# Optimization experiments

Hardware: AMD Instinct MI355X
Metric: run time of the kernel (lower is better)

## Reference

```python
import jax, jax.numpy as jnp
import numpy as np

B, N, IN_F, OUT_F, H = 4, 2048, 128, 128, 4
D = OUT_F // H  # head_dim = 32
NEG_SLOPE = 0.2


def setup_inputs() -> dict:
    key = jax.random.key(0)
    k1, k2, k3, k4, k5 = jax.random.split(key, 5)
    x = jax.random.normal(k1, (B, N, IN_F), dtype=jnp.float32)
    adj = jax.random.randint(k2, (N, N), 0, 2, dtype=jnp.int32)
    adj = adj.at[jnp.arange(N), jnp.arange(N)].set(1)  # self-loops
    # xavier-uniform-like init
    lim_w = float(np.sqrt(6.0 / (IN_F + OUT_F)))
    W = jax.random.uniform(k3, (OUT_F, IN_F), minval=-lim_w, maxval=lim_w, dtype=jnp.float32)
    lim_a = float(np.sqrt(6.0 / (H + D)))
    a_src = jax.random.uniform(k4, (H, D), minval=-lim_a, maxval=lim_a, dtype=jnp.float32)
    a_dst = jax.random.uniform(k5, (H, D), minval=-lim_a, maxval=lim_a, dtype=jnp.float32)
    return {"x": x, "adj": adj, "W": W, "a_src": a_src, "a_dst": a_dst}


def reference(x, adj, W, a_src, a_dst):
    Bx, Nx, _ = x.shape
    # linear projection: (B,N,out) -> (B,N,H,D)
    h = jnp.einsum('bni,oi->bno', x, W).reshape(Bx, Nx, H, D)
    e_src = jnp.einsum('bnhd,hd->bnh', h, a_src)  # (B,N,H)
    e_dst = jnp.einsum('bnhd,hd->bnh', h, a_dst)  # (B,N,H)
    # scores: (B,N_src,H,N_dst)
    scores = jax.nn.leaky_relu(
        e_src[:, :, :, None] + e_dst.transpose(0, 2, 1)[:, None, :, :],
        negative_slope=NEG_SLOPE,
    )
    mask = adj[None, :, None, :]  # (1,N,1,N)
    scores = jnp.where(mask == 0, -jnp.inf, scores)
    attn = jax.nn.softmax(scores, axis=-1)  # (B,N,H,N); dropout is identity at eval
    out = jnp.einsum('bnhm,bmhd->bnhd', attn, h)  # (B,N,H,D)
    return out.reshape(Bx, Nx, H * D)
```

## Files before the change

kernel.cpp:

```cpp
#include <hip/hip_runtime.h>
#include <math.h>

#define BB 4
#define NN 2048
#define FF 128
#define HH 4
#define DD 32
#define NEG_SLOPE 0.2f
#define LOG2E 1.4426950408889634f

typedef __attribute__((ext_vector_type(8))) short short8;
typedef __attribute__((ext_vector_type(4))) float floatx4;
typedef __attribute__((ext_vector_type(2))) float floatx2;

__device__ __forceinline__ float exp2_fast(float x) {
#if __has_builtin(__builtin_amdgcn_exp2f)
    return __builtin_amdgcn_exp2f(x);
#else
    return exp2f(x);
#endif
}

__device__ __forceinline__ int bit_mask(unsigned int w, int bit) {
#if __has_builtin(__builtin_amdgcn_sbfe)
    return __builtin_amdgcn_sbfe((int)w, bit, 1);
#else
    return ((int)(w << (31 - bit))) >> 31;
#endif
}

__device__ __forceinline__ unsigned int pack2_rtne(float lo, float hi) {
    unsigned int ul = __float_as_uint(lo); ul += 0x7FFFu + ((ul >> 16) & 1u);
    unsigned int uh = __float_as_uint(hi); uh += 0x7FFFu + ((uh >> 16) & 1u);
    return (ul >> 16) | (uh & 0xFFFF0000u);
}

__global__ __launch_bounds__(256) void k_prep(const float* __restrict__ x,
                                              const float* __restrict__ W,
                                              const float* __restrict__ a_src,
                                              const float* __restrict__ a_dst,
                                              const int* __restrict__ adj,
                                              unsigned short* __restrict__ ht,
                                              float* __restrict__ es_t,
                                              float* __restrict__ ed_t,
                                              unsigned int* __restrict__ bits) {
    __shared__ unsigned short wbf[128][144];
    __shared__ unsigned short hbf[128][24];
    __shared__ float vs_s[HH][FF], vd_s[HH][FF];
    __shared__ float as_s[FF], ad_s[FF];
    int t = threadIdx.x;

    if (blockIdx.x >= 512) {
        int idx = (blockIdx.x - 512) * 256 + t;
        int n = idx >> 6, w = idx & 63;
        const int4* base = (const int4*)(adj + (size_t)n * NN + w * 32);
        unsigned int word = 0;
#pragma unroll
        for (int q = 0; q < 8; ++q) {
            int4 a = base[q];
            word |= ((unsigned int)(a.x & 1)) << (q * 4 + 0);
            word |= ((unsigned int)(a.y & 1)) << (q * 4 + 1);
            word |= ((unsigned int)(a.z & 1)) << (q * 4 + 2);
            word |= ((unsigned int)(a.w & 1)) << (q * 4 + 3);
        }
        bits[idx] = word;
        return;
    }

    int m0g = blockIdx.x * 16;
    int b = m0g >> 11;
    int m_block = m0g & 2047;

    if (t < FF) { as_s[t] = a_src[t]; ad_s[t] = a_dst[t]; }
#pragma unroll
    for (int k = 0; k < 8; ++k) {
        int idx = t + k * 256;
        int row = idx >> 4, ch = idx & 15;
        const float* wp = W + (size_t)row * FF + ch * 8;
        float4 v0 = *(const float4*)wp;
        float4 v1 = *(const float4*)(wp + 4);
        unsigned int u[4];
        u[0] = pack2_rtne(v0.x, v0.y); u[1] = pack2_rtne(v0.z, v0.w);
        u[2] = pack2_rtne(v1.x, v1.y); u[3] = pack2_rtne(v1.z, v1.w);
        *(int4*)&wbf[row][ch * 8] = *(const int4*)u;
    }
    __syncthreads();

    {
        int i = t & 127;
        float acc4[4] = {0.f, 0.f, 0.f, 0.f};
        if (t < 128) {
            for (int o = 0; o < 128; ++o) {
                float wv = __uint_as_float(((unsigned int)wbf[o][i]) << 16);
                acc4[o >> 5] += wv * as_s[o];
            }
#pragma unroll
            for (int hd = 0; hd < 4; ++hd) vs_s[hd][i] = acc4[hd];
        } else {
            for (int o = 0; o < 128; ++o) {
                float wv = __uint_as_float(((unsigned int)wbf[o][i]) << 16);
                acc4[o >> 5] += wv * ad_s[o];
            }
#pragma unroll
            for (int hd = 0; hd < 4; ++hd) vd_s[hd][i] = acc4[hd];
        }
    }

    int wid = t >> 6, lane = t & 63;
    int r = lane & 15, q = lane >> 4;
    floatx4 acc[2] = {{0.f,0.f,0.f,0.f},{0.f,0.f,0.f,0.f}};
    const float* xrow = x + (size_t)(m0g + r) * FF + q * 8;
#pragma unroll
    for (int kk = 0; kk < 4; ++kk) {
        float4 a0 = *(const float4*)(xrow + kk * 32);
        float4 a1 = *(const float4*)(xrow + kk * 32 + 4);
        union { short8 s8; unsigned int u[4]; } af;
        af.u[0] = pack2_rtne(a0.x, a0.y); af.u[1] = pack2_rtne(a0.z, a0.w);
        af.u[2] = pack2_rtne(a1.x, a1.y); af.u[3] = pack2_rtne(a1.z, a1.w);
#pragma unroll
        for (int c = 0; c < 2; ++c) {
            int o = (wid * 2 + c) * 16 + r;
            short8 bf = *(const short8*)&wbf[o][kk * 32 + q * 8];
            acc[c] = __builtin_amdgcn_mfma_f32_16x16x32_bf16(af.s8, bf, acc[c], 0, 0, 0);
        }
    }
#pragma unroll
    for (int c = 0; c < 2; ++c) {
        int o = (wid * 2 + c) * 16 + r;
        unsigned int u2[2];
        u2[0] = pack2_rtne(acc[c][0], acc[c][1]);
        u2[1] = pack2_rtne(acc[c][2], acc[c][3]);
        *(int2*)&hbf[o][q * 4] = *(const int2*)u2;
    }
    __syncthreads();

    if (t < 128) {
        int hd = t >> 5, d = t & 31;
        unsigned short* op = ht + ((size_t)(b * HH + hd) * DD + d) * NN + m_block;
        *(int4*)op       = *(const int4*)&hbf[t][0];
        *(int4*)(op + 8) = *(const int4*)&hbf[t][8];
    }
    {
        int m = t >> 4, sg = t & 15;
        const float* xp = x + (size_t)(m0g + m) * FF + sg * 8;
        float4 x0 = *(const float4*)xp;
        float4 x1 = *(const float4*)(xp + 4);
#pragma unroll
        for (int hd = 0; hd < 4; ++hd) {
            const float* vsp = &vs_s[hd][sg * 8];
            const float* vdp = &vd_s[hd][sg * 8];
            float es = x0.x * vsp[0] + x0.y * vsp[1] + x0.z * vsp[2] + x0.w * vsp[3]
                     + x1.x * vsp[4] + x1.y * vsp[5] + x1.z * vsp[6] + x1.w * vsp[7];
            float ed = x0.x * vdp[0] + x0.y * vdp[1] + x0.z * vdp[2] + x0.w * vdp[3]
                     + x1.x * vdp[4] + x1.y * vdp[5] + x1.z * vdp[6] + x1.w * vdp[7];
#pragma unroll
            for (int k = 1; k < 16; k <<= 1) {
                es += __shfl_xor(es, k);
                ed += __shfl_xor(ed, k);
            }
            if (sg == 0) {
                size_t eb = (size_t)(b * HH + hd) * NN + m_block + m;
                es_t[eb] = es * LOG2E;
                ed_t[eb] = ed * LOG2E;
            }
        }
    }
}

__global__ __launch_bounds__(512) void k_attn(
        const unsigned short* __restrict__ ht,
        const unsigned int* __restrict__ bits,
        const float* __restrict__ es_t,
        const float* __restrict__ ed_t,
        float* __restrict__ out) {
    __shared__ float ep[NN * 2];
    int t = threadIdx.x;
    int n0 = blockIdx.x * 64;
    int bh = blockIdx.y;
    int b = bh >> 2, head = bh & 3;

    int wid = t >> 6, lane = t & 63;
    int q = lane >> 4, r = lane & 15;
    int qo = q * 8;
    int half = wid >> 2, wsub = wid & 3;
    int n_l = wsub * 16 + r;

    {
        float4 v = ((const float4*)(ed_t + (size_t)bh * NN))[t];
        float4 o01, o23;
        o01.x = exp2_fast(v.x); o01.y = exp2_fast(NEG_SLOPE * v.x);
        o01.z = exp2_fast(v.y); o01.w = exp2_fast(NEG_SLOPE * v.y);
        o23.x = exp2_fast(v.z); o23.y = exp2_fast(NEG_SLOPE * v.z);
        o23.z = exp2_fast(v.w); o23.w = exp2_fast(NEG_SLOPE * v.w);
        ((float4*)ep)[2 * t]     = o01;
        ((float4*)ep)[2 * t + 1] = o23;
    }
    float esv = es_t[(size_t)bh * NN + n0 + n_l];
    floatx2 es2 = {exp2_fast(esv), exp2_fast(NEG_SLOPE * esv)};
    __syncthreads();

    floatx4 acc0 = {0.f, 0.f, 0.f, 0.f};
    floatx4 acc1 = {0.f, 0.f, 0.f, 0.f};
    floatx4 accd = {0.f, 0.f, 0.f, 0.f};
    union { short8 s8; int i[4]; } ones;
    ones.i[0] = 0x3F803F80; ones.i[1] = 0x3F803F80;
    ones.i[2] = 0x3F803F80; ones.i[3] = 0x3F803F80;

    const float* eph = ep + half * 2048;
    const unsigned short* hrow0 = ht + (size_t)bh * DD * NN
                                  + (size_t)r * NN + half * 1024 + qo;
    const unsigned short* hrow1 = hrow0 + 16 * NN;
    const unsigned int* bp = bits + (size_t)(n0 + n_l) * 64 + half * 32;

#pragma unroll
    for (int g = 0; g < 8; ++g) {
        int4 bwv = *(const int4*)(bp + g * 4);
#pragma unroll
        for (int c = 0; c < 4; ++c) {
            unsigned int word = (unsigned int)((&bwv.x)[c]);
            int mb = (g * 4 + c) * 32;
            unsigned int wq = word >> qo;
            const float* pbase = eph + (mb + qo) * 2;
            union { short8 s8; int i[4]; } af;
#pragma unroll
            for (int jp = 0; jp < 4; ++jp) {
                float4 d2 = *(const float4*)(pbase + jp * 4);
                floatx2 p0 = es2 * (floatx2){d2.x, d2.y};
                floatx2 p1 = es2 * (floatx2){d2.z, d2.w};
                float w0 = fmaxf(p0.x, p0.y);
                float w1 = fmaxf(p1.x, p1.y);
                int m0 = bit_mask(wq, 2 * jp);
                int m1 = bit_mask(wq, 2 * jp + 1);
                w0 = __uint_as_float(__float_as_uint(w0) & (unsigned int)m0);
                w1 = __uint_as_float(__float_as_uint(w1) & (unsigned int)m1);
                af.i[jp] = __builtin_amdgcn_perm(__float_as_uint(w1),
                                                 __float_as_uint(w0),
                                                 0x07060302u);
            }
            short8 b0 = *(const short8*)(hrow0 + mb);
            short8 b1 = *(const short8*)(hrow1 + mb);
            acc0 = __builtin_amdgcn_mfma_f32_16x16x32_bf16(af.s8, b0, acc0, 0, 0, 0);
            acc1 = __builtin_amdgcn_mfma_f32_16x16x32_bf16(af.s8, b1, acc1, 0, 0, 0);
            accd = __builtin_amdgcn_mfma_f32_16x16x32_bf16(af.s8, ones.s8, accd, 0, 0, 0);
        }
    }

    __syncthreads();
    float* scr = ep;
    if (half == 1) {
        int base = (wsub * 64 + lane) * 12;
        *(floatx4*)&scr[base + 0] = acc0;
        *(floatx4*)&scr[base + 4] = acc1;
        *(floatx4*)&scr[base + 8] = accd;
    }
    __syncthreads();
    if (half == 0) {
        int base = (wsub * 64 + lane) * 12;
        floatx4 p0 = *(const floatx4*)&scr[base + 0];
        floatx4 p1 = *(const floatx4*)&scr[base + 4];
        floatx4 pd = *(const floatx4*)&scr[base + 8];
#pragma unroll
        for (int k = 0; k < 4; ++k) {
            acc0[k] += p0[k]; acc1[k] += p1[k]; accd[k] += pd[k];
        }
#pragma unroll
        for (int reg = 0; reg < 4; ++reg) {
            int nrow = n0 + wsub * 16 + q * 4 + reg;
            float inv = 1.0f / accd[reg];
            float* op = out + ((size_t)(b * NN + nrow)) * FF + head * DD;
            op[r]      = acc0[reg] * inv;
            op[16 + r] = acc1[reg] * inv;
        }
    }
}

extern "C" void kernel_launch(void* const* d_in, const int* in_sizes, int n_in,
                              void* d_out, int out_size, void* d_ws, size_t ws_size,
                              hipStream_t stream) {
    const float* x     = (const float*)d_in[0];
    const int*   adj   = (const int*)d_in[1];
    const float* W     = (const float*)d_in[2];
    const float* a_src = (const float*)d_in[3];
    const float* a_dst = (const float*)d_in[4];
    float* out = (float*)d_out;

    float* es_t = (float*)d_ws;
    float* ed_t = es_t + (size_t)BB * HH * NN;
    unsigned int* bits = (unsigned int*)(ed_t + (size_t)BB * HH * NN);
    unsigned short* ht = (unsigned short*)(bits + (size_t)NN * (NN / 32));

    hipLaunchKernelGGL(k_prep, dim3(1024), dim3(256), 0, stream,
                       x, W, a_src, a_dst, adj, ht, es_t, ed_t, bits);
    hipLaunchKernelGGL(k_attn, dim3(NN / 64, BB * HH), dim3(512), 0, stream,
                       ht, bits, es_t, ed_t, out);
}
```

Before: 115.2 us.

## Stage V tiles in LDS, precompute exp2 of dst scores in prep kernel

The attention kernel now stages the bf16 value rows in padded shared-memory chunks, with a sync-separated reload per chunk, instead of reading short8 fragments straight from global memory. The exp2 of the destination scores and of their leaky-slope scaled form moves into the prep kernel, which writes interleaved pairs, so each attention block only copies them. The per-row leaky-relu max is rewritten as fmax(d.x, tn*d.y), with tn = exp2(-0.8*es), which drops one multiply per element. In exchange the kernel adds about 33KB of LDS, which may lower occupancy, plus eight extra barriers, and the chunk reloads are not overlapped with compute.

After: 98.27 us. -14.7%, faster.

```diff
diff --git a/kernel.cpp b/kernel.cpp
--- a/kernel.cpp
+++ b/kernel.cpp
@@ -161,18 +161,25 @@
             if (sg == 0) {
                 size_t eb = (size_t)(b * HH + hd) * NN + m_block + m;
                 es_t[eb] = es * LOG2E;
-                ed_t[eb] = ed * LOG2E;
-            }
-        }
-    }
-}
-
+                float ee = ed * LOG2E;
+                float2 pr;
+                pr.x = exp2_fast(ee);
+                pr.y = exp2_fast(NEG_SLOPE * ee);
+                *(float2*)(ed_t + eb * 2) = pr;
+            }
+        }
+    }
+}
+
+#define HBW 528
+#define HOF 264
 __global__ __launch_bounds__(512) void k_attn(
         const unsigned short* __restrict__ ht,
         const unsigned int* __restrict__ bits,
         const float* __restrict__ es_t,
         const float* __restrict__ ed_t,
         float* __restrict__ out) {
+    __shared__ unsigned short hb[DD * HBW];
     __shared__ float ep[NN * 2];
     int t = threadIdx.x;
     int n0 = blockIdx.x * 64;
@@ -185,18 +192,23 @@
     int half = wid >> 2, wsub = wid & 3;
     int n_l = wsub * 16 + r;
 
+    const unsigned short* htp = ht + (size_t)bh * DD * NN;
+
     {
-        float4 v = ((const float4*)(ed_t + (size_t)bh * NN))[t];
-        float4 o01, o23;
-        o01.x = exp2_fast(v.x); o01.y = exp2_fast(NEG_SLOPE * v.x);
-        o01.z = exp2_fast(v.y); o01.w = exp2_fast(NEG_SLOPE * v.y);
-        o23.x = exp2_fast(v.z); o23.y = exp2_fast(NEG_SLOPE * v.z);
-        o23.z = exp2_fast(v.w); o23.w = exp2_fast(NEG_SLOPE * v.w);
-        ((float4*)ep)[2 * t]     = o01;
-        ((float4*)ep)[2 * t + 1] = o23;
+        const float4* src = (const float4*)(ed_t + (size_t)bh * NN * 2);
+        ((float4*)ep)[t]       = src[t];
+        ((float4*)ep)[t + 512] = src[t + 512];
+    }
+#pragma unroll
+    for (int k2 = 0; k2 < 4; ++k2) {
+        int j = t + k2 * 512;
+        int hf = j >> 10, jj = j & 1023;
+        int d = jj >> 5, c16 = jj & 31;
+        int4 v = *(const int4*)(htp + (size_t)d * NN + hf * 1024 + c16 * 8);
+        *(int4*)&hb[d * HBW + hf * HOF + c16 * 8] = v;
     }
     float esv = es_t[(size_t)bh * NN + n0 + n_l];
-    floatx2 es2 = {exp2_fast(esv), exp2_fast(NEG_SLOPE * esv)};
+    float tn = exp2_fast(-0.8f * esv);
     __syncthreads();
 
     floatx4 acc0 = {0.f, 0.f, 0.f, 0.f};
@@ -206,47 +218,61 @@
     ones.i[0] = 0x3F803F80; ones.i[1] = 0x3F803F80;
     ones.i[2] = 0x3F803F80; ones.i[3] = 0x3F803F80;
 
-    const float* eph = ep + half * 2048;
-    const unsigned short* hrow0 = ht + (size_t)bh * DD * NN
-                                  + (size_t)r * NN + half * 1024 + qo;
-    const unsigned short* hrow1 = hrow0 + 16 * NN;
-    const unsigned int* bp = bits + (size_t)(n0 + n_l) * 64 + half * 32;
-
-#pragma unroll
-    for (int g = 0; g < 8; ++g) {
-        int4 bwv = *(const int4*)(bp + g * 4);
-#pragma unroll
-        for (int c = 0; c < 4; ++c) {
-            unsigned int word = (unsigned int)((&bwv.x)[c]);
-            int mb = (g * 4 + c) * 32;
-            unsigned int wq = word >> qo;
-            const float* pbase = eph + (mb + qo) * 2;
-            union { short8 s8; int i[4]; } af;
-#pragma unroll
-            for (int jp = 0; jp < 4; ++jp) {
-                float4 d2 = *(const float4*)(pbase + jp * 4);
-                floatx2 p0 = es2 * (floatx2){d2.x, d2.y};
-                floatx2 p1 = es2 * (floatx2){d2.z, d2.w};
-                float w0 = fmaxf(p0.x, p0.y);
-                float w1 = fmaxf(p1.x, p1.y);
-                int m0 = bit_mask(wq, 2 * jp);
-                int m1 = bit_mask(wq, 2 * jp + 1);
-                w0 = __uint_as_float(__float_as_uint(w0) & (unsigned int)m0);
-                w1 = __uint_as_float(__float_as_uint(w1) & (unsigned int)m1);
-                af.i[jp] = __builtin_amdgcn_perm(__float_as_uint(w1),
-                                                 __float_as_uint(w0),
-                                                 0x07060302u);
-            }
-            short8 b0 = *(const short8*)(hrow0 + mb);
-            short8 b1 = *(const short8*)(hrow1 + mb);
-            acc0 = __builtin_amdgcn_mfma_f32_16x16x32_bf16(af.s8, b0, acc0, 0, 0, 0);
-            acc1 = __builtin_amdgcn_mfma_f32_16x16x32_bf16(af.s8, b1, acc1, 0, 0, 0);
-            accd = __builtin_amdgcn_mfma_f32_16x16x32_bf16(af.s8, ones.s8, accd, 0, 0, 0);
-        }
-    }
-
-    __syncthreads();
-    float* scr = ep;
+    const unsigned short* hrow0 = &hb[r * HBW + half * HOF + qo];
+    const unsigned short* hrow1 = &hb[(r + 16) * HBW + half * HOF + qo];
+    const unsigned int* bpb = bits + (size_t)(n0 + n_l) * 64 + half * 32;
+
+    for (int ck = 0; ck < 4; ++ck) {
+        int4 bw0 = *(const int4*)(bpb + ck * 8);
+        int4 bw1 = *(const int4*)(bpb + ck * 8 + 4);
+        const float* pb_ck = ep + (half * 1024 + ck * 256) * 2;
+#pragma unroll
+        for (int g = 0; g < 2; ++g) {
+            int4 bwv = g ? bw1 : bw0;
+#pragma unroll
+            for (int c = 0; c < 4; ++c) {
+                unsigned int word = (unsigned int)((&bwv.x)[c]);
+                int mb = g * 128 + c * 32;
+                unsigned int wq = word >> qo;
+                const float* pbase = pb_ck + (mb + qo) * 2;
+                union { short8 s8; int i[4]; } af;
+#pragma unroll
+                for (int jp = 0; jp < 4; ++jp) {
+                    float4 d2 = *(const float4*)(pbase + jp * 4);
+                    float w0 = fmaxf(d2.x, tn * d2.y);
+                    float w1 = fmaxf(d2.z, tn * d2.w);
+                    int m0 = bit_mask(wq, 2 * jp);
+                    int m1 = bit_mask(wq, 2 * jp + 1);
+                    w0 = __uint_as_float(__float_as_uint(w0) & (unsigned int)m0);
+                    w1 = __uint_as_float(__float_as_uint(w1) & (unsigned int)m1);
+                    af.i[jp] = __builtin_amdgcn_perm(__float_as_uint(w1),
+                                                     __float_as_uint(w0),
+                                                     0x07060302u);
+                }
+                short8 b0 = *(const short8*)(hrow0 + mb);
+                short8 b1 = *(const short8*)(hrow1 + mb);
+                acc0 = __builtin_amdgcn_mfma_f32_16x16x32_bf16(af.s8, b0, acc0, 0, 0, 0);
+                acc1 = __builtin_amdgcn_mfma_f32_16x16x32_bf16(af.s8, b1, acc1, 0, 0, 0);
+                accd = __builtin_amdgcn_mfma_f32_16x16x32_bf16(af.s8, ones.s8, accd, 0, 0, 0);
+            }
+        }
+        __syncthreads();
+        if (ck < 3) {
+            int ckn = ck + 1;
+#pragma unroll
+            for (int k2 = 0; k2 < 4; ++k2) {
+                int j = t + k2 * 512;
+                int hf = j >> 10, jj = j & 1023;
+                int d = jj >> 5, c16 = jj & 31;
+                int4 v = *(const int4*)(htp + (size_t)d * NN + hf * 1024
+                                        + ckn * 256 + c16 * 8);
+                *(int4*)&hb[d * HBW + hf * HOF + c16 * 8] = v;
+            }
+        }
+        __syncthreads();
+    }
+
+    float* scr = (float*)hb;
     if (half == 1) {
         int base = (wsub * 64 + lane) * 12;
         *(floatx4*)&scr[base + 0] = acc0;
@@ -286,7 +312,7 @@
 
     float* es_t = (float*)d_ws;
     float* ed_t = es_t + (size_t)BB * HH * NN;
-    unsigned int* bits = (unsigned int*)(ed_t + (size_t)BB * HH * NN);
+    unsigned int* bits = (unsigned int*)(ed_t + (size_t)BB * HH * NN * 2);
     unsigned short* ht = (unsigned short*)(bits + (size_t)NN * (NN / 32));
 
     hipLaunchKernelGGL(k_prep, dim3(1024), dim3(256), 0, stream,
```
